# Optimization experiments

Hardware: AMD Instinct MI355X
Metric: run time of the kernel (lower is better)

The kernel has to match this reference:

```python
import jax, jax.numpy as jnp
import numpy as np

B, CZ, E, V, H, W = 256, 512, 512, 4096, 16, 16  # batch, z_channels, embed_dim, vocab, latent HxW


def setup_inputs() -> dict:
    key = jax.random.key(0)
    k0, k1, k2, k3 = jax.random.split(key, 4)
    x = jax.random.normal(k0, (B, CZ, H, W), jnp.float32)          # encoder feature map
    pre_w = jax.random.normal(k1, (E, CZ), jnp.float32) * 0.02     # 1x1 pre_quant_conv weight
    pre_b = jnp.zeros((E,), jnp.float32)
    emb = jax.random.uniform(k2, (V, E), jnp.float32, -1.0 / V, 1.0 / V)  # codebook, uniform init as in module
    post_w = jax.random.normal(k3, (CZ, E), jnp.float32) * 0.02    # 1x1 post_quant_conv weight
    post_b = jnp.zeros((CZ,), jnp.float32)
    return dict(x=x, pre_w=pre_w, pre_b=pre_b, emb=emb, post_w=post_w, post_b=post_b)


def reference(x, pre_w, pre_b, emb, post_w, post_b):
    # pre_quant_conv: 1x1 Conv2d(CZ -> E)
    z = jnp.einsum('bchw,ec->behw', x, pre_w) + pre_b[None, :, None, None]
    b, e, h, w = z.shape
    # flatten spatial: (b h w, e)
    zf = z.transpose(0, 2, 3, 1).reshape(-1, e)
    # expanded squared-distance to codebook: ||z||^2 + ||c||^2 - 2 z.c
    dist = (jnp.sum(zf * zf, axis=1, keepdims=True)
            + jnp.sum(emb * emb, axis=1)
            - 2.0 * zf @ emb.T)                                    # [bhw, V]
    tokens = jnp.argmin(dist, axis=-1)                             # [bhw] int
    z_q = emb[tokens].reshape(b, h, w, e).transpose(0, 3, 1, 2)    # gather -> [b,e,h,w]
    # straight-through estimator
    dec_in = z + jax.lax.stop_gradient(z_q - z)
    # post_quant_conv: 1x1 Conv2d(E -> CZ)
    rec = jnp.einsum('behw,ce->bchw', dec_in, post_w) + post_b[None, :, None, None]
    return z, z_q, rec
```

## Files before the change

kernel.cpp:

```cpp
#include <hip/hip_runtime.h>
#include <hip/hip_bf16.h>

typedef unsigned short u16;
typedef unsigned int   u32;
typedef unsigned long long u64;

using short8 = __attribute__((ext_vector_type(8))) short;
using f32x4  = __attribute__((ext_vector_type(4))) float;
using u16x8  = __attribute__((ext_vector_type(8))) unsigned short;

#define AS_GLOBAL __attribute__((address_space(1)))
#define AS_LDS    __attribute__((address_space(3)))

__device__ __forceinline__ u16 f2b(float x){
  u32 u = __float_as_uint(x);
  u32 r = (u + 0x7FFFu + ((u >> 16) & 1u)) >> 16;
  return (u16)r;
}
__device__ __forceinline__ float b2f(u16 h){ return __uint_as_float(((u32)h) << 16); }

__device__ __forceinline__ void gload16(u16* l, const u16* g){
  __builtin_amdgcn_global_load_lds((const AS_GLOBAL u32*)g, (AS_LDS u32*)l, 16, 0, 0);
}

__device__ __forceinline__ u64 umin64(u64 a, u64 b){ return a < b ? a : b; }

__device__ __forceinline__ u64 shfl_xor_u64(u64 v, int m){
  u32 lo = __shfl_xor((u32)v, m, 64);
  u32 hi = __shfl_xor((u32)(v >> 32), m, 64);
  return ((u64)hi << 32) | lo;
}

__global__ void k_cvt(const float* __restrict__ w, u16* __restrict__ d, int n){
  int i = blockIdx.x * 256 + threadIdx.x;
  if (i < n) d[i] = f2b(w[i]);
}

__global__ void k_cnorm(const float* __restrict__ emb, float* __restrict__ cnorm){
  int v = blockIdx.x, lane = threadIdx.x;
  const float* r = emb + (size_t)v * 512;
  float s = 0.f;
  #pragma unroll
  for (int i = 0; i < 8; ++i){ float x = r[lane + i * 64]; s += x * x; }
  #pragma unroll
  for (int off = 32; off; off >>= 1) s += __shfl_down(s, off, 64);
  if (lane == 0) cnorm[v] = s;
}

__global__ void k_tcvt(const float* __restrict__ src, u16* __restrict__ d){
  __shared__ float t[64][65];
  const int bid = blockIdx.x;
  const int b  = bid >> 5;
  const int rb = (bid >> 2) & 7;
  const int cb = bid & 3;
  const float* s = src + ((size_t)b * 512 + (size_t)rb * 64) * 256 + cb * 64;
  const int tid = threadIdx.x;
  #pragma unroll
  for (int j = 0; j < 4; ++j){
    int fl = j * 256 + tid;
    int r = fl >> 4, c4 = (fl & 15) * 4;
    float4 v = *(const float4*)(s + (size_t)r * 256 + c4);
    t[r][c4 + 0] = v.x; t[r][c4 + 1] = v.y; t[r][c4 + 2] = v.z; t[r][c4 + 3] = v.w;
  }
  __syncthreads();
  u16* o = d + ((size_t)b * 256 + (size_t)cb * 64) * 512 + rb * 64;
  #pragma unroll
  for (int j = 0; j < 2; ++j){
    int fl = j * 256 + tid;
    int c = fl >> 3, r8 = (fl & 7) * 8;
    u16x8 hv;
    #pragma unroll
    for (int i = 0; i < 8; ++i) hv[i] = f2b(t[r8 + i][c]);
    *(u16x8*)(o + (size_t)c * 512 + r8) = hv;
  }
}

__global__ void k_zq(const u64* __restrict__ keys, const float* __restrict__ emb, float* __restrict__ zq){
  int sidx = blockIdx.x * 64 + threadIdx.x;
  int b = sidx >> 8, s = sidx & 255;
  int v = (int)(u32)keys[sidx];
  const float4* er = (const float4*)(emb + (size_t)v * 512);
  float* o = zq + (size_t)b * 512 * 256 + s;
  #pragma unroll 4
  for (int e4 = 0; e4 < 128; ++e4){
    float4 vv = er[e4];
    o[(size_t)(e4 * 4 + 0) * 256] = vv.x;
    o[(size_t)(e4 * 4 + 1) * 256] = vv.y;
    o[(size_t)(e4 * 4 + 2) * 256] = vv.z;
    o[(size_t)(e4 * 4 + 3) * 256] = vv.w;
  }
}

template<int MODE>
__global__ __launch_bounds__(256, 4) void k_gemm(
    const u16* __restrict__ Ah,
    const u16* __restrict__ Bh,
    const u64* __restrict__ gkeys,
    const float* __restrict__ bias,
    const float* __restrict__ cnorm,
    float* __restrict__ Cout,
    u64* __restrict__ okeys,
    int M, int mtbits)
{
  constexpr int K = 512;
  __shared__ __align__(16) u16 sA[128 * 64];
  __shared__ __align__(16) u16 sB[128 * 64];

  const int tid  = threadIdx.x;
  const int lane = tid & 63;
  const int wid  = tid >> 6;
  const int wm = wid >> 1, wn = wid & 1;

  const int nwg = gridDim.x;
  const int chunk = nwg >> 3;
  const int pb = blockIdx.x;
  const int bid = (pb & 7) * chunk + (pb >> 3);

  const int mt = bid & ((1 << mtbits) - 1);
  const int nt = (bid >> mtbits) & 1;
  const int b  = bid >> (mtbits + 1);
  const int m0 = mt * 128;
  const int n0 = nt * 128;
  const int bbase = b * 256;

  const u16* ga[4];
  const u16* gb[4];
  int ldso[4];
  #pragma unroll
  for (int i = 0; i < 4; ++i){
    int e = i * 256 + tid;
    int r = e >> 3;
    int sl = (e & 7) ^ (r & 7);
    ldso[i] = e * 8;
    ga[i] = Ah + (size_t)(m0 + r) * K + sl * 8;
    size_t brow;
    if (MODE == 2) brow = (size_t)(u32)gkeys[bbase + n0 + r];
    else           brow = (size_t)(bbase + n0 + r);
    gb[i] = Bh + brow * K + sl * 8;
  }

  const f32x4 zero4 = {0.f, 0.f, 0.f, 0.f};
  f32x4 acc[4][4];
  #pragma unroll
  for (int i = 0; i < 4; ++i)
    #pragma unroll
    for (int j = 0; j < 4; ++j) acc[i][j] = zero4;

  int aoff[2][4], boff[2][4];
  #pragma unroll
  for (int ks = 0; ks < 2; ++ks)
    #pragma unroll
    for (int f = 0; f < 4; ++f){
      int rA = wm * 64 + f * 16 + (lane & 15);
      aoff[ks][f] = rA * 64 + (((ks * 4 + (lane >> 4)) ^ (rA & 7)) * 8);
      int rB = wn * 64 + f * 16 + (lane & 15);
      boff[ks][f] = rB * 64 + (((ks * 4 + (lane >> 4)) ^ (rB & 7)) * 8);
    }

  for (int kt = 0; kt < 8; ++kt){
    const int k0 = kt * 64;
    #pragma unroll
    for (int i = 0; i < 4; ++i){
      gload16(&sA[ldso[i]], ga[i] + k0);
      gload16(&sB[ldso[i]], gb[i] + k0);
    }
    __syncthreads();
    #pragma unroll
    for (int ks = 0; ks < 2; ++ks){
      short8 ah[4], bh[4];
      #pragma unroll
      for (int f = 0; f < 4; ++f){
        ah[f] = *(const short8*)&sA[aoff[ks][f]];
        bh[f] = *(const short8*)&sB[boff[ks][f]];
      }
      #pragma unroll
      for (int fm = 0; fm < 4; ++fm)
        #pragma unroll
        for (int fn = 0; fn < 4; ++fn)
          acc[fm][fn] = __builtin_amdgcn_mfma_f32_16x16x32_bf16(ah[fm], bh[fn], acc[fm][fn], 0, 0, 0);
    }
    __syncthreads();
  }

  if (MODE != 1){
    const int row0 = m0 + wm * 64;
    const int col  = n0 + wn * 64 + (lane & 15);
    float* Cb = Cout + (size_t)b * M * 256;
    #pragma unroll
    for (int fm = 0; fm < 4; ++fm){
      #pragma unroll
      for (int j = 0; j < 4; ++j){
        int row = row0 + fm * 16 + (lane >> 4) * 4 + j;
        float bi = bias[row];
        #pragma unroll
        for (int fn = 0; fn < 4; ++fn)
          Cb[(size_t)row * 256 + col + fn * 16] = acc[fm][fn][j] + bi;
      }
    }
  } else {
    u64 best[4];
    #pragma unroll
    for (int fn = 0; fn < 4; ++fn){
      u64 bk = ~0ull;
      #pragma unroll
      for (int fm = 0; fm < 4; ++fm){
        #pragma unroll
        for (int j = 0; j < 4; ++j){
          int v = m0 + wm * 64 + fm * 16 + (lane >> 4) * 4 + j;
          float sc = cnorm[v] - 2.0f * acc[fm][fn][j];
          u32 o = __float_as_uint(sc);
          o = (o & 0x80000000u) ? ~o : (o | 0x80000000u);
          u64 key = ((u64)o << 32) | (u32)v;
          bk = umin64(bk, key);
        }
      }
      bk = umin64(bk, shfl_xor_u64(bk, 16));
      bk = umin64(bk, shfl_xor_u64(bk, 32));
      best[fn] = bk;
    }
    __syncthreads();
    u64* kbuf = (u64*)&sA[0];
    if (lane < 16){
      #pragma unroll
      for (int fn = 0; fn < 4; ++fn)
        kbuf[wm * 128 + wn * 64 + fn * 16 + lane] = best[fn];
    }
    __syncthreads();
    if (tid < 128){
      u64 k2 = umin64(kbuf[tid], kbuf[128 + tid]);
      atomicMin((unsigned long long*)(okeys + (size_t)bbase + n0 + tid), (unsigned long long)k2);
    }
  }
}

extern "C" void kernel_launch(void* const* d_in, const int* in_sizes, int n_in,
                              void* d_out, int out_size, void* d_ws, size_t ws_size,
                              hipStream_t stream){
  const float* x      = (const float*)d_in[0];
  const float* pre_w  = (const float*)d_in[1];
  const float* pre_b  = (const float*)d_in[2];
  const float* emb    = (const float*)d_in[3];
  const float* post_w = (const float*)d_in[4];
  const float* post_b = (const float*)d_in[5];

  float* z_out   = (float*)d_out;
  float* zq_out  = z_out + 33554432;
  float* rec_out = z_out + 67108864;

  char* w = (char*)d_ws;
  u16* prew_b  = (u16*)(w);
  u16* postw_b = (u16*)(w + 524288);
  u16* emb_b   = (u16*)(w + 1048576);
  float* cnorm = (float*)(w + 5242880);
  u64* keys    = (u64*)(w + 5259264);
  u16* xb      = (u16*)(w + 5783552);
  u16* zb = xb;

  k_cvt  <<<1024, 256, 0, stream>>>(pre_w, prew_b, 262144);
  k_cvt  <<<1024, 256, 0, stream>>>(post_w, postw_b, 262144);
  k_cvt  <<<8192, 256, 0, stream>>>(emb, emb_b, 2097152);
  k_cnorm<<<4096, 64, 0, stream>>>(emb, cnorm);
  hipMemsetAsync(keys, 0xFF, 65536 * sizeof(u64), stream);

  k_tcvt<<<8192, 256, 0, stream>>>(x, xb);

  k_gemm<0><<<256 * 2 * 4, 256, 0, stream>>>(prew_b, xb,
      nullptr, pre_b, nullptr, z_out, nullptr, 512, 2);

  k_tcvt<<<8192, 256, 0, stream>>>(z_out, zb);

  k_gemm<1><<<256 * 2 * 32, 256, 0, stream>>>(emb_b, zb,
      nullptr, nullptr, cnorm, nullptr, keys, 4096, 5);

  k_zq<<<1024, 64, 0, stream>>>(keys, emb, zq_out);

  k_gemm<2><<<256 * 2 * 4, 256, 0, stream>>>(postw_b, emb_b,
      keys, post_b, nullptr, rec_out, nullptr, 512, 2);
}
```

Baseline: 592.6 us.

## Replace codebook distance GEMM with 256x256 double-buffered pipelined kernel

The distance/argmin GEMM moves from a 128x128-tile, 4-wave kernel that loads and then syncs each K step to a new 512-thread kernel. The new kernel uses 256x256 tiles, 8 waves and a double-buffered LDS ping-pong. Global-to-LDS loads for upcoming K slices are issued in quarter-tile pieces between MFMA phases, using explicit vmcnt waits, barriers and setprio to overlap memory with compute. The larger tile halves the reads of the codebook and activations and the number of atomicMin operations, at the cost of 128 KiB LDS and more accumulator registers per wave.

```diff
diff --git a/kernel.cpp b/kernel.cpp
--- a/kernel.cpp
+++ b/kernel.cpp
@@ -30,6 +30,9 @@
   u32 hi = __shfl_xor((u32)(v >> 32), m, 64);
   return ((u64)hi << 32) | lo;
 }
+
+__device__ __forceinline__ void waitv4(){ asm volatile("s_waitcnt vmcnt(4)" ::: "memory"); }
+__device__ __forceinline__ void waitv0(){ asm volatile("s_waitcnt vmcnt(0)" ::: "memory"); }
 
 __global__ void k_cvt(const float* __restrict__ w, u16* __restrict__ d, int n){
   int i = blockIdx.x * 256 + threadIdx.x;
@@ -197,40 +200,189 @@
           Cb[(size_t)row * 256 + col + fn * 16] = acc[fm][fn][j] + bi;
       }
     }
-  } else {
-    u64 best[4];
-    #pragma unroll
-    for (int fn = 0; fn < 4; ++fn){
-      u64 bk = ~0ull;
-      #pragma unroll
-      for (int fm = 0; fm < 4; ++fm){
-        #pragma unroll
-        for (int j = 0; j < 4; ++j){
-          int v = m0 + wm * 64 + fm * 16 + (lane >> 4) * 4 + j;
-          float sc = cnorm[v] - 2.0f * acc[fm][fn][j];
-          u32 o = __float_as_uint(sc);
-          o = (o & 0x80000000u) ? ~o : (o | 0x80000000u);
-          u64 key = ((u64)o << 32) | (u32)v;
-          bk = umin64(bk, key);
-        }
-      }
-      bk = umin64(bk, shfl_xor_u64(bk, 16));
-      bk = umin64(bk, shfl_xor_u64(bk, 32));
-      best[fn] = bk;
-    }
-    __syncthreads();
-    u64* kbuf = (u64*)&sA[0];
-    if (lane < 16){
-      #pragma unroll
-      for (int fn = 0; fn < 4; ++fn)
-        kbuf[wm * 128 + wn * 64 + fn * 16 + lane] = best[fn];
-    }
-    __syncthreads();
-    if (tid < 128){
-      u64 k2 = umin64(kbuf[tid], kbuf[128 + tid]);
-      atomicMin((unsigned long long*)(okeys + (size_t)bbase + n0 + tid), (unsigned long long)k2);
-    }
-  }
+  }
+}
+
+__global__ __launch_bounds__(512, 2) void k_gemm2(
+    const u16* __restrict__ Ah,
+    const u16* __restrict__ Bh,
+    const float* __restrict__ cnorm,
+    u64* __restrict__ okeys)
+{
+  __shared__ __align__(16) u16 lds[2][32768];
+
+  const int tid  = threadIdx.x;
+  const int lane = tid & 63;
+  const int wid  = tid >> 6;
+  const int wm   = wid >> 2;
+  const int wn   = wid & 3;
+
+  const int nwg = gridDim.x;
+  const int chunk = nwg >> 3;
+  const int pb  = blockIdx.x;
+  const int bid = (pb & 7) * chunk + (pb >> 3);
+  const int mt = bid & 15;
+  const int b  = bid >> 4;
+  const int m0 = mt * 256;
+  const int bbase = b * 256;
+
+  const int l8 = lane >> 3;
+  const int sl = (lane & 7) ^ l8;
+  const int arb = (wid < 4) ? wid * 16 : 128 + (wid - 4) * 16;
+  const int brb = (wid >> 1) * 64 + (wid & 1) * 16;
+
+  const u16* srcA0 = Ah + (size_t)(m0 + arb + l8) * 512 + sl * 8;
+  const u16* srcA1 = srcA0 + 8 * 512;
+  const u16* srcB0 = Bh + (size_t)(bbase + brb + l8) * 512 + sl * 8;
+  const u16* srcB1 = srcB0 + 8 * 512;
+  const int dA0 = arb * 64 + lane * 8;
+  const int dA1 = dA0 + 512;
+  const int dB0 = 16384 + brb * 64 + lane * 8;
+  const int dB1 = dB0 + 512;
+
+#define STG_AFML(p, kk) { gload16(&lds[p][dA0], srcA0 + (kk)); gload16(&lds[p][dA1], srcA1 + (kk)); }
+#define STG_AFMH(p, kk) { gload16(&lds[p][dA0 + 4096], srcA0 + 32768 + (kk)); gload16(&lds[p][dA1 + 4096], srcA1 + 32768 + (kk)); }
+#define STG_BFNL(p, kk) { gload16(&lds[p][dB0], srcB0 + (kk)); gload16(&lds[p][dB1], srcB1 + (kk)); }
+#define STG_BFNH(p, kk) { gload16(&lds[p][dB0 + 2048], srcB0 + 16384 + (kk)); gload16(&lds[p][dB1 + 2048], srcB1 + 16384 + (kk)); }
+
+  int aoff[2][8], boff[2][4];
+  #pragma unroll
+  for (int ks = 0; ks < 2; ++ks){
+    #pragma unroll
+    for (int f = 0; f < 8; ++f){
+      int rA = wm * 128 + f * 16 + (lane & 15);
+      aoff[ks][f] = rA * 64 + (((ks * 4 + (lane >> 4)) ^ (rA & 7)) * 8);
+    }
+    #pragma unroll
+    for (int f = 0; f < 4; ++f){
+      int rB = wn * 64 + f * 16 + (lane & 15);
+      boff[ks][f] = 16384 + rB * 64 + (((ks * 4 + (lane >> 4)) ^ (rB & 7)) * 8);
+    }
+  }
+
+  const f32x4 zero4 = {0.f, 0.f, 0.f, 0.f};
+  f32x4 acc[8][4];
+  #pragma unroll
+  for (int i = 0; i < 8; ++i)
+    #pragma unroll
+    for (int j = 0; j < 4; ++j) acc[i][j] = zero4;
+
+  STG_AFML(0, 0) STG_AFMH(0, 0) STG_BFNL(0, 0) STG_BFNH(0, 0)
+  STG_AFML(1, 64) STG_BFNH(1, 64)
+  waitv4();
+  __builtin_amdgcn_s_barrier();
+  __builtin_amdgcn_sched_barrier(0);
+
+  for (int t = 0; t < 8; ++t){
+    const int bc = t & 1;
+    const int bn = bc ^ 1;
+    const u16* cb = &lds[bc][0];
+    const int kn1 = (t + 1) * 64, kn2 = (t + 2) * 64;
+    short8 ah[4][2], bh[2][2];
+
+    if (t < 7) STG_AFMH(bn, kn1)
+    #pragma unroll
+    for (int f = 0; f < 4; ++f){ ah[f][0] = *(const short8*)&cb[aoff[0][f]]; ah[f][1] = *(const short8*)&cb[aoff[1][f]]; }
+    #pragma unroll
+    for (int f = 0; f < 2; ++f){ bh[f][0] = *(const short8*)&cb[boff[0][f]]; bh[f][1] = *(const short8*)&cb[boff[1][f]]; }
+    __builtin_amdgcn_s_setprio(1);
+    #pragma unroll
+    for (int fm = 0; fm < 4; ++fm)
+      #pragma unroll
+      for (int fn = 0; fn < 2; ++fn){
+        acc[fm][fn] = __builtin_amdgcn_mfma_f32_16x16x32_bf16(ah[fm][0], bh[fn][0], acc[fm][fn], 0, 0, 0);
+        acc[fm][fn] = __builtin_amdgcn_mfma_f32_16x16x32_bf16(ah[fm][1], bh[fn][1], acc[fm][fn], 0, 0, 0);
+      }
+    __builtin_amdgcn_s_setprio(0);
+    __builtin_amdgcn_sched_barrier(0);
+    __builtin_amdgcn_s_barrier();
+    __builtin_amdgcn_sched_barrier(0);
+
+    if (t < 7) STG_BFNL(bn, kn1)
+    #pragma unroll
+    for (int f = 0; f < 2; ++f){ bh[f][0] = *(const short8*)&cb[boff[0][2 + f]]; bh[f][1] = *(const short8*)&cb[boff[1][2 + f]]; }
+    __builtin_amdgcn_s_setprio(1);
+    #pragma unroll
+    for (int fm = 0; fm < 4; ++fm)
+      #pragma unroll
+      for (int fn = 0; fn < 2; ++fn){
+        acc[fm][2 + fn] = __builtin_amdgcn_mfma_f32_16x16x32_bf16(ah[fm][0], bh[fn][0], acc[fm][2 + fn], 0, 0, 0);
+        acc[fm][2 + fn] = __builtin_amdgcn_mfma_f32_16x16x32_bf16(ah[fm][1], bh[fn][1], acc[fm][2 + fn], 0, 0, 0);
+      }
+    __builtin_amdgcn_s_setprio(0);
+    __builtin_amdgcn_sched_barrier(0);
+    __builtin_amdgcn_s_barrier();
+    __builtin_amdgcn_sched_barrier(0);
+
+    if (t < 6) STG_AFML(bc, kn2)
+    #pragma unroll
+    for (int f = 0; f < 4; ++f){ ah[f][0] = *(const short8*)&cb[aoff[0][4 + f]]; ah[f][1] = *(const short8*)&cb[aoff[1][4 + f]]; }
+    __builtin_amdgcn_s_setprio(1);
+    #pragma unroll
+    for (int fm = 0; fm < 4; ++fm)
+      #pragma unroll
+      for (int fn = 0; fn < 2; ++fn){
+        acc[4 + fm][2 + fn] = __builtin_amdgcn_mfma_f32_16x16x32_bf16(ah[fm][0], bh[fn][0], acc[4 + fm][2 + fn], 0, 0, 0);
+        acc[4 + fm][2 + fn] = __builtin_amdgcn_mfma_f32_16x16x32_bf16(ah[fm][1], bh[fn][1], acc[4 + fm][2 + fn], 0, 0, 0);
+      }
+    __builtin_amdgcn_s_setprio(0);
+    __builtin_amdgcn_sched_barrier(0);
+    __builtin_amdgcn_s_barrier();
+    __builtin_amdgcn_sched_barrier(0);
+
+    if (t < 6) STG_BFNH(bc, kn2)
+    #pragma unroll
+    for (int f = 0; f < 2; ++f){ bh[f][0] = *(const short8*)&cb[boff[0][f]]; bh[f][1] = *(const short8*)&cb[boff[1][f]]; }
+    __builtin_amdgcn_s_setprio(1);
+    #pragma unroll
+    for (int fm = 0; fm < 4; ++fm)
+      #pragma unroll
+      for (int fn = 0; fn < 2; ++fn){
+        acc[4 + fm][fn] = __builtin_amdgcn_mfma_f32_16x16x32_bf16(ah[fm][0], bh[fn][0], acc[4 + fm][fn], 0, 0, 0);
+        acc[4 + fm][fn] = __builtin_amdgcn_mfma_f32_16x16x32_bf16(ah[fm][1], bh[fn][1], acc[4 + fm][fn], 0, 0, 0);
+      }
+    __builtin_amdgcn_s_setprio(0);
+    __builtin_amdgcn_sched_barrier(0);
+    if (t < 6) waitv4(); else if (t == 6) waitv0();
+    __builtin_amdgcn_s_barrier();
+    __builtin_amdgcn_sched_barrier(0);
+  }
+
+  __syncthreads();
+  u64 best[4];
+  #pragma unroll
+  for (int fn = 0; fn < 4; ++fn){
+    u64 bk = ~0ull;
+    #pragma unroll
+    for (int fm = 0; fm < 8; ++fm){
+      #pragma unroll
+      for (int j = 0; j < 4; ++j){
+        int v = m0 + wm * 128 + fm * 16 + (lane >> 4) * 4 + j;
+        float sc = cnorm[v] - 2.0f * acc[fm][fn][j];
+        u32 o = __float_as_uint(sc);
+        o = (o & 0x80000000u) ? ~o : (o | 0x80000000u);
+        bk = umin64(bk, ((u64)o << 32) | (u32)v);
+      }
+    }
+    bk = umin64(bk, shfl_xor_u64(bk, 16));
+    bk = umin64(bk, shfl_xor_u64(bk, 32));
+    best[fn] = bk;
+  }
+  u64* kbuf = (u64*)&lds[0][0];
+  if (lane < 16){
+    #pragma unroll
+    for (int fn = 0; fn < 4; ++fn)
+      kbuf[wm * 256 + wn * 64 + fn * 16 + lane] = best[fn];
+  }
+  __syncthreads();
+  if (tid < 256){
+    u64 k2 = umin64(kbuf[tid], kbuf[256 + tid]);
+    atomicMin((unsigned long long*)(okeys + bbase + tid), (unsigned long long)k2);
+  }
+#undef STG_AFML
+#undef STG_AFMH
+#undef STG_BFNL
+#undef STG_BFNH
 }
 
 extern "C" void kernel_launch(void* const* d_in, const int* in_sizes, int n_in,
@@ -269,8 +421,7 @@
 
   k_tcvt<<<8192, 256, 0, stream>>>(z_out, zb);
 
-  k_gemm<1><<<256 * 2 * 32, 256, 0, stream>>>(emb_b, zb,
-      nullptr, nullptr, cnorm, nullptr, keys, 4096, 5);
+  k_gemm2<<<256 * 16, 512, 0, stream>>>(emb_b, zb, cnorm, keys);
 
   k_zq<<<1024, 64, 0, stream>>>(keys, emb, zq_out);
 
```

Result: faster. 548.9 us (-7.4%).
